# Kernel optimization log

Measured on AMD Instinct MI355X. Metric: run time of the kernel, lower is better.

Reference implementation:

```python
import jax, jax.numpy as jnp
import numpy as np

H = 32          # num attention heads
KVH = 8         # num kv heads
D = 64          # head dim
HID = 2048      # hidden size
MAXB = 1024     # max_bias_length
BASE = 10000.0  # rope theta


def _rope(x, pos):
    # x: (B, S, h, D), pos: (S,) -- GPT-NeoX half-split rotary
    half = D // 2
    inv_freq = 1.0 / (BASE ** (jnp.arange(0, D, 2, dtype=jnp.float32) / D))  # (half,)
    ang = pos[:, None].astype(jnp.float32) * inv_freq                         # (S, half)
    cos = jnp.cos(ang)[None, :, None, :]
    sin = jnp.sin(ang)[None, :, None, :]
    x1, x2 = x[..., :half], x[..., half:]
    return jnp.concatenate([x1 * cos - x2 * sin, x2 * cos + x1 * sin], axis=-1)


def setup_inputs() -> dict:
    key = jax.random.key(0)
    ks = jax.random.split(key, 7)
    B, S = 2, 1024
    hidden_states = jax.random.normal(ks[0], (B, S, HID), dtype=jnp.float32)
    attention_mask = jnp.broadcast_to(
        jnp.tril(jnp.ones((S, S), dtype=jnp.int32))[None, None], (B, 1, S, S))
    # weights stored as (in, out): y = x @ W  (same math as torch Linear)
    Wq = jax.random.normal(ks[1], (HID, H * D), dtype=jnp.float32) * 0.02
    Wk = jax.random.normal(ks[2], (HID, KVH * D), dtype=jnp.float32) * 0.02
    Wv = jax.random.normal(ks[3], (HID, KVH * D), dtype=jnp.float32) * 0.02
    Wo = jax.random.normal(ks[4], (H * D, HID), dtype=jnp.float32) * 0.02
    bias_diag = jax.random.normal(ks[5], (H, MAXB), dtype=jnp.float32) * 0.001
    softmax_offset = jnp.zeros((H,), dtype=jnp.float32)
    return {"hidden_states": hidden_states, "attention_mask": attention_mask,
            "Wq": Wq, "Wk": Wk, "Wv": Wv, "Wo": Wo,
            "bias_diag": bias_diag, "softmax_offset": softmax_offset}


def reference(hidden_states, attention_mask, Wq, Wk, Wv, Wo, bias_diag, softmax_offset):
    B, S, _ = hidden_states.shape
    scaling = D ** (-0.5)
    pos = jnp.arange(S)

    q = (hidden_states @ Wq).reshape(B, S, H, D)
    k = (hidden_states @ Wk).reshape(B, S, KVH, D)
    v = (hidden_states @ Wv).reshape(B, S, KVH, D)

    q = _rope(q, pos)
    k = _rope(k, pos)

    # (B, H, S, D); repeat_kv via repeat on head axis
    q = q.transpose(0, 2, 1, 3)
    k = jnp.repeat(k.transpose(0, 2, 1, 3), H // KVH, axis=1)
    v = jnp.repeat(v.transpose(0, 2, 1, 3), H // KVH, axis=1)

    scores = jnp.einsum('bhqd,bhkd->bhqk', q, k) * scaling

    # learnable diagonal relative-position bias
    rel = pos[:, None] - pos[None, :]                     # (S, S)
    valid = ((rel >= 0) & (rel < MAXB)).astype(scores.dtype)
    idx = jnp.clip(rel, 0, MAXB - 1)
    bias = bias_diag[:, idx] * valid                      # (H, S, S)
    scores = scores + bias[None]

    scores = jnp.where(attention_mask[:, :, :, :S] == 0, -jnp.inf, scores)

    weights = jax.nn.softmax(scores.astype(jnp.float32), axis=-1)

    # adaptive offset subtraction + relu
    offset = jnp.abs(softmax_offset + 1.0)[None, :, None, None]
    num_visible = (pos + 1).astype(jnp.float32)[None, None, :, None]  # along query dim
    weights = jax.nn.relu(weights - offset / num_visible)

    attn_out = jnp.einsum('bhqk,bhkd->bhqd', weights.astype(v.dtype), v)
    attn_out = attn_out.transpose(0, 2, 1, 3).reshape(B, S, H * D)
    return attn_out @ Wo
```

## Files before the change

kernel.cpp:

```cpp
#include <hip/hip_runtime.h>
#include <cstdint>
#include <cstddef>

#define BB   2
#define SS   1024
#define HID  2048
#define HH   32
#define KVHH 8
#define DD   64
#define NQKV 3072
#define QKW  2560

typedef __attribute__((ext_vector_type(8))) short bf16x8;
typedef __attribute__((ext_vector_type(4))) float f32x4;
typedef __attribute__((ext_vector_type(4))) unsigned int u32x4;

__device__ __forceinline__ unsigned short f2bf(float f) {
    unsigned int u = __float_as_uint(f);
    unsigned int r = (u + 0x7fffu + ((u >> 16) & 1u)) >> 16;
    return (unsigned short)r;
}

__device__ __forceinline__ float ex2(float x) {
    float r; asm("v_exp_f32 %0, %1" : "=v"(r) : "v"(x)); return r;
}

__device__ __forceinline__ void g2l16(const unsigned short* g, unsigned short* l) {
    __builtin_amdgcn_global_load_lds(
        (__attribute__((address_space(1))) void*)(unsigned short*)g,
        (__attribute__((address_space(3))) void*)l,
        16, 0, 0);
}

__global__ __launch_bounds__(256) void prep(
    const float* __restrict__ hidden,
    const float* __restrict__ Wq, const float* __restrict__ Wk,
    const float* __restrict__ Wv, const float* __restrict__ Wo,
    unsigned short* __restrict__ hidden_bf,
    unsigned short* __restrict__ WqkvT,
    unsigned short* __restrict__ WoT)
{
    const int z   = blockIdx.z;
    const int tid = threadIdx.x;

    if (z == 4) {
        int r0 = blockIdx.y * 64, c0 = blockIdx.x * 64;
        #pragma unroll
        for (int p = 0; p < 4; ++p) {
            int f = tid + p * 256;
            int row = r0 + (f >> 4), c4 = c0 + (f & 15) * 4;
            float4 v = *(const float4*)&hidden[(size_t)row * 2048 + c4];
            ushort4 o;
            o.x = f2bf(v.x); o.y = f2bf(v.y); o.z = f2bf(v.z); o.w = f2bf(v.w);
            *(ushort4*)&hidden_bf[(size_t)row * 2048 + c4] = o;
        }
        return;
    }

    const float* W;
    unsigned short* Wt;
    int N;
    if (z == 0)      { W = Wq; Wt = WqkvT;                        N = 2048; }
    else if (z == 1) { W = Wk; Wt = WqkvT + (size_t)2048 * 2048;  N = 512;  }
    else if (z == 2) { W = Wv; Wt = WqkvT + (size_t)2560 * 2048;  N = 512;  }
    else             { W = Wo; Wt = WoT;                          N = 2048; }
    if (blockIdx.x * 64 >= N) return;

    __shared__ float t[64][68];
    const int n0 = blockIdx.x * 64, k0 = blockIdx.y * 64;
    #pragma unroll
    for (int p = 0; p < 4; ++p) {
        int f = tid + p * 256;
        int row = f >> 4, c4 = (f & 15) * 4;
        float4 v = *(const float4*)&W[(size_t)(k0 + row) * N + n0 + c4];
        t[row][c4 + 0] = v.x; t[row][c4 + 1] = v.y;
        t[row][c4 + 2] = v.z; t[row][c4 + 3] = v.w;
    }
    __syncthreads();
    #pragma unroll
    for (int p = 0; p < 4; ++p) {
        int f = tid + p * 256;
        int nrow = f >> 4, kc4 = (f & 15) * 4;
        ushort4 o;
        o.x = f2bf(t[kc4 + 0][nrow]);
        o.y = f2bf(t[kc4 + 1][nrow]);
        o.z = f2bf(t[kc4 + 2][nrow]);
        o.w = f2bf(t[kc4 + 3][nrow]);
        *(ushort4*)&Wt[(size_t)(n0 + nrow) * 2048 + k0 + kc4] = o;
    }
}

__global__ __launch_bounds__(256) void gemm_qkv_fused(
    const unsigned short* __restrict__ A,
    const unsigned short* __restrict__ Bt,
    unsigned short* __restrict__ qk_bf,
    unsigned short* __restrict__ v_t)
{
    __shared__ __align__(16) char smem[49152];
    float* Ctf = (float*)smem;

    const int tid  = threadIdx.x;
    const int lane = tid & 63;
    const int wave = tid >> 6;
    const int quad = lane >> 4;
    const int l15  = lane & 15;
    const int wm = (wave >> 1) * 64, wn = (wave & 1) * 32;
    const int m0 = blockIdx.y * 128, n0 = blockIdx.x * 64;
    const int K = 2048;

    f32x4 acc[4][2] = {};

#define STAGE_Q(k0s, buf) do {                                                \
    unsigned short* Ad = (unsigned short*)(smem + (buf) * 24576);             \
    unsigned short* Bd = (unsigned short*)(smem + (buf) * 24576 + 16384);     \
    _Pragma("unroll")                                                         \
    for (int p = 0; p < 4; ++p) {                                             \
        int ci = tid + p * 256;                                               \
        int row_ = ci >> 3, sc_ = (ci & 7) ^ (row_ & 7);                      \
        g2l16(&A[(size_t)(m0 + row_) * K + (k0s) + sc_ * 8], Ad + ci * 8);    \
    }                                                                         \
    _Pragma("unroll")                                                         \
    for (int p = 0; p < 2; ++p) {                                             \
        int ci = tid + p * 256;                                               \
        int row_ = ci >> 3, sc_ = (ci & 7) ^ (row_ & 7);                      \
        g2l16(&Bt[(size_t)(n0 + row_) * K + (k0s) + sc_ * 8], Bd + ci * 8);   \
    } } while (0)

    STAGE_Q(0, 0);
    __syncthreads();
    int cur = 0;
    for (int k0 = 0; k0 < K; k0 += 64) {
        if (k0 + 64 < K) STAGE_Q(k0 + 64, cur ^ 1);
        const short* Ab = (const short*)(smem + cur * 24576);
        const short* Bb = (const short*)(smem + cur * 24576 + 16384);

        #pragma unroll
        for (int s = 0; s < 2; ++s) {
            bf16x8 af[4], bfr[2];
            #pragma unroll
            for (int i = 0; i < 4; ++i) {
                int row = wm + i * 16 + l15;
                af[i] = *(const bf16x8*)(Ab + row * 64 +
                        ((((s << 2) | quad) ^ (row & 7)) * 8));
            }
            #pragma unroll
            for (int j = 0; j < 2; ++j) {
                int row = wn + j * 16 + l15;
                bfr[j] = *(const bf16x8*)(Bb + row * 64 +
                        ((((s << 2) | quad) ^ (row & 7)) * 8));
            }
            #pragma unroll
            for (int i = 0; i < 4; ++i)
                #pragma unroll
                for (int j = 0; j < 2; ++j)
                    acc[i][j] = __builtin_amdgcn_mfma_f32_16x16x32_bf16(
                        af[i], bfr[j], acc[i][j], 0, 0, 0);
        }
        __syncthreads();
        cur ^= 1;
    }

    #pragma unroll
    for (int i = 0; i < 4; ++i)
        #pragma unroll
        for (int j = 0; j < 2; ++j)
            #pragma unroll
            for (int rg = 0; rg < 4; ++rg)
                Ctf[(wm + i * 16 + quad * 4 + rg) * 65 + wn + j * 16 + l15]
                    = acc[i][j][rg];
    __syncthreads();

    const int bx = blockIdx.x;
    const int b  = m0 >> 10;
    const int s0 = m0 & 1023;

    if (bx < 40) {
        const int hc = bx * 64;
        const float scale = (bx < 32) ? 0.18033688011112042f : 1.0f;
        #pragma unroll
        for (int p = 0; p < 4; ++p) {
            int idx = tid + p * 256;
            int row = idx >> 3, t0 = (idx & 7) * 4;
            int s = s0 + row;
            ushort4 o1, o2;
            #pragma unroll
            for (int k = 0; k < 4; ++k) {
                int t = t0 + k;
                float x1 = Ctf[row * 65 + t];
                float x2 = Ctf[row * 65 + t + 32];
                float inv = __expf(-(float)t * 0.28782313662425572f);
                float ang = (float)s * inv;
                float c  = __cosf(ang);
                float sn = __sinf(ang);
                ((unsigned short*)&o1)[k] = f2bf((x1 * c - x2 * sn) * scale);
                ((unsigned short*)&o2)[k] = f2bf((x2 * c + x1 * sn) * scale);
            }
            unsigned short* dst = qk_bf + (size_t)(m0 + row) * QKW + hc;
            *(ushort4*)&dst[t0]      = o1;
            *(ushort4*)&dst[t0 + 32] = o2;
        }
    } else {
        const int vb = b * 512 + (bx - 40) * 64;
        #pragma unroll
        for (int p = 0; p < 8; ++p) {
            int idx = tid + p * 256;
            int c = idx >> 5, srow = (idx & 31) * 4;
            ushort4 o;
            #pragma unroll
            for (int k = 0; k < 4; ++k)
                ((unsigned short*)&o)[k] = f2bf(Ctf[(srow + k) * 65 + c]);
            *(ushort4*)&v_t[(size_t)(vb + c) * 1024 + s0 + srow] = o;
        }
    }
#undef STAGE_Q
}

__global__ __launch_bounds__(256) void gemm_bf16_bt(
    const unsigned short* __restrict__ A,
    const unsigned short* __restrict__ Bt,
    float* __restrict__ C, int M, int N, int K)
{
    __shared__ __align__(16) char smem[49152];

    const int tid  = threadIdx.x;
    const int lane = tid & 63;
    const int wave = tid >> 6;
    const int quad = lane >> 4;
    const int l15  = lane & 15;
    const int wm = (wave >> 1) * 64, wn = (wave & 1) * 32;
    const int m0 = blockIdx.y * 128, n0 = blockIdx.x * 64;

    f32x4 acc[4][2] = {};

#define STAGE_O(k0s, buf) do {                                                \
    unsigned short* Ad = (unsigned short*)(smem + (buf) * 24576);             \
    unsigned short* Bd = (unsigned short*)(smem + (buf) * 24576 + 16384);     \
    _Pragma("unroll")                                                         \
    for (int p = 0; p < 4; ++p) {                                             \
        int ci = tid + p * 256;                                               \
        int row_ = ci >> 3, sc_ = (ci & 7) ^ (row_ & 7);                      \
        g2l16(&A[(size_t)(m0 + row_) * K + (k0s) + sc_ * 8], Ad + ci * 8);    \
    }                                                                         \
    _Pragma("unroll")                                                         \
    for (int p = 0; p < 2; ++p) {                                             \
        int ci = tid + p * 256;                                               \
        int row_ = ci >> 3, sc_ = (ci & 7) ^ (row_ & 7);                      \
        g2l16(&Bt[(size_t)(n0 + row_) * K + (k0s) + sc_ * 8], Bd + ci * 8);   \
    } } while (0)

    STAGE_O(0, 0);
    __syncthreads();
    int cur = 0;
    for (int k0 = 0; k0 < K; k0 += 64) {
        if (k0 + 64 < K) STAGE_O(k0 + 64, cur ^ 1);
        const short* Ab = (const short*)(smem + cur * 24576);
        const short* Bb = (const short*)(smem + cur * 24576 + 16384);

        #pragma unroll
        for (int s = 0; s < 2; ++s) {
            bf16x8 af[4], bfr[2];
            #pragma unroll
            for (int i = 0; i < 4; ++i) {
                int row = wm + i * 16 + l15;
                af[i] = *(const bf16x8*)(Ab + row * 64 +
                        ((((s << 2) | quad) ^ (row & 7)) * 8));
            }
            #pragma unroll
            for (int j = 0; j < 2; ++j) {
                int row = wn + j * 16 + l15;
                bfr[j] = *(const bf16x8*)(Bb + row * 64 +
                        ((((s << 2) | quad) ^ (row & 7)) * 8));
            }
            #pragma unroll
            for (int i = 0; i < 4; ++i)
                #pragma unroll
                for (int j = 0; j < 2; ++j)
                    acc[i][j] = __builtin_amdgcn_mfma_f32_16x16x32_bf16(
                        af[i], bfr[j], acc[i][j], 0, 0, 0);
        }
        __syncthreads();
        cur ^= 1;
    }

    #pragma unroll
    for (int i = 0; i < 4; ++i) {
        int grow = m0 + wm + i * 16 + quad * 4;
        #pragma unroll
        for (int j = 0; j < 2; ++j) {
            int gcol = n0 + wn + j * 16 + l15;
            #pragma unroll
            for (int rg = 0; rg < 4; ++rg)
                C[(size_t)(grow + rg) * N + gcol] = acc[i][j][rg];
        }
    }
#undef STAGE_O
}

__global__ __launch_bounds__(512, 8) void attn_mfma(
    const unsigned short* __restrict__ qk_bf,
    const unsigned short* __restrict__ v_t,
    const float* __restrict__ bias_diag,
    const float* __restrict__ soff,
    unsigned short* __restrict__ AO)
{
    static const unsigned char qtab[16] =
        {15, 14, 13, 12, 10, 11, 8, 9, 4, 5, 6, 7, 1, 0, 3, 2};
    const int id = (int)blockIdx.x;
    const int vq = id >> 8;
    const int c  = id & 255;
    const int qt = qtab[(vq << 2) | (c & 3)];
    const int bh = c >> 2;
    const int h  = bh & 31;
    const int b  = bh >> 5;
    const int kh = h >> 2;
    const int tid  = threadIdx.x;
    const int lane = tid & 63;
    const int wave = tid >> 6;
    const int grp  = wave >> 2;
    const int w4   = wave & 3;
    const int quad = lane >> 4;
    const int l15  = lane & 15;
    const int q0   = qt * 64;

    __shared__ short Ks[2][4096];
    __shared__ short Vs[2][4096];
    __shared__ float bd_s[1024];
    __shared__ float red[2][64];
    float* Fred = (float*)&Ks[0][0];

    for (int i = tid; i < 1024; i += 512)
        bd_s[i] = bias_diag[h * 1024 + i] * 1.4426950408889634f;

    const unsigned short* Kg = qk_bf + (size_t)(b * SS) * QKW + 2048 + kh * 64;
    const unsigned short* Vg = v_t + (size_t)(b * 512 + kh * 64) * SS;

    const int qrow = q0 + w4 * 16 + l15;

    const unsigned short* Qg =
        qk_bf + (size_t)(b * SS + q0 + w4 * 16) * QKW + h * 64;
    bf16x8 qf0 = *(const bf16x8*)(Qg + (size_t)l15 * QKW + quad * 8);
    bf16x8 qf1 = *(const bf16x8*)(Qg + (size_t)l15 * QKW + 32 + quad * 8);

#define STAGE_K(j, buf) do {                                                  \
    int ci = tid;                                                             \
    int row_ = ci >> 3, sc_ = (ci & 7) ^ (row_ & 7);                          \
    g2l16(Kg + (size_t)((j) * 64 + row_) * QKW + sc_ * 8,                     \
          (unsigned short*)&Ks[buf][ci * 8]);                                 \
} while (0)

#define STAGE_V(j, buf) do {                                                  \
    int ci = tid;                                                             \
    int row_ = ci >> 3, sc_ = (ci & 7) ^ (row_ & 7);                          \
    g2l16(Vg + (size_t)row_ * SS + (j) * 64 + sc_ * 8,                        \
          (unsigned short*)&Vs[buf][ci * 8]);                                 \
} while (0)

    float lpa[4] = {0.f, 0.f, 0.f, 0.f};
    STAGE_K(0, 0);
    __syncthreads();
    int cur = 0;
    for (int j = 0; j <= qt; ++j) {
        if (j < qt) STAGE_K(j + 1, cur ^ 1);
        const short* Kb = Ks[cur];
        const bool diag = (j == qt);

        f32x4 acc[2] = {};
        #pragma unroll
        for (int nn = 0; nn < 2; ++nn) {
            int nb = 2 * grp + nn;
            if (diag && nb > w4) continue;
            int row = nb * 16 + l15, sw = row & 7;
            bf16x8 a0 = *(const bf16x8*)(Kb + row * 64 + ((quad ^ sw) * 8));
            bf16x8 a1 = *(const bf16x8*)(Kb + row * 64 + (((quad + 4) ^ sw) * 8));
            acc[nn] = __builtin_amdgcn_mfma_f32_16x16x32_bf16(a0, qf0, acc[nn], 0, 0, 0);
            acc[nn] = __builtin_amdgcn_mfma_f32_16x16x32_bf16(a1, qf1, acc[nn], 0, 0, 0);
        }
        if (!diag) {
            #pragma unroll
            for (int nn = 0; nn < 2; ++nn) {
                int rel0 = qrow - (j * 64 + (2 * grp + nn) * 16 + quad * 4);
                #pragma unroll
                for (int r = 0; r < 4; ++r)
                    lpa[r] += ex2(acc[nn][r] + bd_s[rel0 - r]);
            }
        } else {
            #pragma unroll
            for (int nn = 0; nn < 2; ++nn) {
                int nb = 2 * grp + nn;
                if (nb > w4) continue;
                #pragma unroll
                for (int r = 0; r < 4; ++r) {
                    int rel = qrow - (j * 64 + nb * 16 + quad * 4 + r);
                    if (rel >= 0) lpa[r] += ex2(acc[nn][r] + bd_s[rel]);
                }
            }
        }
        __syncthreads();
        cur ^= 1;
    }

    float lp = (lpa[0] + lpa[1]) + (lpa[2] + lpa[3]);
    lp += __shfl_xor(lp, 16, 64);
    lp += __shfl_xor(lp, 32, 64);
    if (quad == 0) red[grp][w4 * 16 + l15] = lp;
    __syncthreads();
    lp = red[0][w4 * 16 + l15] + red[1][w4 * 16 + l15];
    const float invl = 1.f / lp;
    const float cl   = fabsf(soff[h] + 1.f) / (float)(qrow + 1) * lp;

    f32x4 oacc[4] = {};
    STAGE_K(0, 0);
    STAGE_V(0, 0);
    __syncthreads();
    cur = 0;
    for (int j = 0; j <= qt; ++j) {
        if (j < qt) { STAGE_K(j + 1, cur ^ 1); STAGE_V(j + 1, cur ^ 1); }
        const short* Kb = Ks[cur];
        const short* Vb = Vs[cur];
        const bool diag = (j == qt);

        f32x4 acc[2] = {};
        #pragma unroll
        for (int nn = 0; nn < 2; ++nn) {
            int nb = 2 * grp + nn;
            if (diag && nb > w4) continue;
            int row = nb * 16 + l15, sw = row & 7;
            bf16x8 a0 = *(const bf16x8*)(Kb + row * 64 + ((quad ^ sw) * 8));
            bf16x8 a1 = *(const bf16x8*)(Kb + row * 64 + (((quad + 4) ^ sw) * 8));
            acc[nn] = __builtin_amdgcn_mfma_f32_16x16x32_bf16(a0, qf0, acc[nn], 0, 0, 0);
            acc[nn] = __builtin_amdgcn_mfma_f32_16x16x32_bf16(a1, qf1, acc[nn], 0, 0, 0);
        }

        unsigned int pk[2][2];
        if (!diag) {
            #pragma unroll
            for (int nn = 0; nn < 2; ++nn) {
                float w[4];
                int rel0 = qrow - (j * 64 + (2 * grp + nn) * 16 + quad * 4);
                #pragma unroll
                for (int r = 0; r < 4; ++r)
                    w[r] = fmaxf(ex2(acc[nn][r] + bd_s[rel0 - r]) - cl, 0.f);
                asm("v_cvt_pk_bf16_f32 %0, %1, %2" : "=v"(pk[nn][0]) : "v"(w[0]), "v"(w[1]));
                asm("v_cvt_pk_bf16_f32 %0, %1, %2" : "=v"(pk[nn][1]) : "v"(w[2]), "v"(w[3]));
            }
        } else {
            #pragma unroll
            for (int nn = 0; nn < 2; ++nn) {
                int nb = 2 * grp + nn;
                float w[4];
                #pragma unroll
                for (int r = 0; r < 4; ++r) {
                    int rel = qrow - (j * 64 + nb * 16 + quad * 4 + r);
                    float e = 0.f;
                    if (rel >= 0)
                        e = fmaxf(ex2(acc[nn][r] + bd_s[rel]) - cl, 0.f);
                    w[r] = e;
                }
                asm("v_cvt_pk_bf16_f32 %0, %1, %2" : "=v"(pk[nn][0]) : "v"(w[0]), "v"(w[1]));
                asm("v_cvt_pk_bf16_f32 %0, %1, %2" : "=v"(pk[nn][1]) : "v"(w[2]), "v"(w[3]));
            }
        }
        unsigned int ppk[2][2];
        #pragma unroll
        for (int nn = 0; nn < 2; ++nn) {
            ppk[nn][0] = __shfl_xor(pk[nn][0], 16, 64);
            ppk[nn][1] = __shfl_xor(pk[nn][1], 16, 64);
        }

        if (!(diag && grp == 1 && w4 < 2)) {
            const bool oddq = quad & 1;
            const int  cv   = ((quad & 1) << 1) | (quad >> 1);
            unsigned int w0 = oddq ? ppk[1][0] : pk[0][0];
            unsigned int w1 = oddq ? ppk[1][1] : pk[0][1];
            unsigned int w2 = oddq ? pk[1][0]  : ppk[0][0];
            unsigned int w3 = oddq ? pk[1][1]  : ppk[0][1];
            u32x4 t; t[0] = w0; t[1] = w1; t[2] = w2; t[3] = w3;
            bf16x8 pf = __builtin_bit_cast(bf16x8, t);
            #pragma unroll
            for (int nd = 0; nd < 4; ++nd) {
                int rowv = nd * 16 + l15, swv = rowv & 7;
                bf16x8 vf = *(const bf16x8*)(Vb + rowv * 64 + (((cv + 4 * grp) ^ swv) * 8));
                oacc[nd] = __builtin_amdgcn_mfma_f32_16x16x32_bf16(pf, vf, oacc[nd], 0, 0, 0);
            }
        }
        __syncthreads();
        cur ^= 1;
    }

    if (grp == 1) {
        #pragma unroll
        for (int nd = 0; nd < 4; ++nd)
            #pragma unroll
            for (int r = 0; r < 4; ++r)
                Fred[(w4 * 16 + quad * 4 + r) * 64 + nd * 16 + l15] = oacc[nd][r];
    }
    __syncthreads();
    if (grp == 0) {
        float invl_r[4];
        #pragma unroll
        for (int r = 0; r < 4; ++r)
            invl_r[r] = __shfl(invl, quad * 4 + r, 64);
        unsigned short* aop =
            AO + (size_t)(b * SS + q0 + w4 * 16 + quad * 4) * 2048 + h * 64 + l15;
        #pragma unroll
        for (int nd = 0; nd < 4; ++nd)
            #pragma unroll
            for (int r = 0; r < 4; ++r) {
                float o = (oacc[nd][r] +
                           Fred[(w4 * 16 + quad * 4 + r) * 64 + nd * 16 + l15])
                          * invl_r[r];
                aop[(size_t)r * 2048 + nd * 16] = f2bf(o);
            }
    }
#undef STAGE_K
#undef STAGE_V
}

extern "C" void kernel_launch(void* const* d_in, const int* in_sizes, int n_in,
                              void* d_out, int out_size, void* d_ws, size_t ws_size,
                              hipStream_t stream)
{
    const float* hidden    = (const float*)d_in[0];
    const float* Wq        = (const float*)d_in[2];
    const float* Wk        = (const float*)d_in[3];
    const float* Wv        = (const float*)d_in[4];
    const float* Wo        = (const float*)d_in[5];
    const float* bias_diag = (const float*)d_in[6];
    const float* soff      = (const float*)d_in[7];
    float* out = (float*)d_out;

    char* wsb = (char*)d_ws;
    unsigned short* hidden_bf = (unsigned short*)wsb;
    unsigned short* WqkvT     = (unsigned short*)(wsb + (size_t)8388608);
    unsigned short* AO_bf     = (unsigned short*)(wsb + (size_t)12582912);
    unsigned short* WoT       = (unsigned short*)(wsb + (size_t)20971520);
    unsigned short* qk_bf     = (unsigned short*)(wsb + (size_t)29360128);
    unsigned short* v_t       = (unsigned short*)(wsb + (size_t)29360128 + (size_t)2048 * 2560 * 2);

    prep<<<dim3(32, 32, 5), dim3(256), 0, stream>>>(
        hidden, Wq, Wk, Wv, Wo, hidden_bf, WqkvT, WoT);

    gemm_qkv_fused<<<dim3(48, 16), dim3(256), 0, stream>>>(
        hidden_bf, WqkvT, qk_bf, v_t);

    attn_mfma<<<dim3(1024), dim3(512), 0, stream>>>(
        qk_bf, v_t, bias_diag, soff, AO_bf);

    gemm_bf16_bt<<<dim3(2048 / 64, 2048 / 128), dim3(256), 0, stream>>>(
        AO_bf, WoT, out, 2048, 2048, 2048);
}
```

Measured before the change: 197.1 us.

## Use persistent attention blocks with atomic work queue and MFMA priority hints

Converts the attention kernel into a persistent kernel with 768 blocks that pull work items from a global atomic counter. The counter is reset by the prep kernel. Items are ordered longest query tile first, so the causal triangle balances dynamically instead of relying on a static interleave table. It also wraps the MFMA sections in s_setprio and lowers the launch-bounds occupancy hint from 8 to 6. The cost is extra barriers and an atomic per item, and correctness now depends on the reset in prep running before every launch.

Result: slower. 207.4 us (+5.3%).

```diff
diff --git a/kernel.cpp b/kernel.cpp
--- a/kernel.cpp
+++ b/kernel.cpp
@@ -38,12 +38,14 @@
     const float* __restrict__ Wv, const float* __restrict__ Wo,
     unsigned short* __restrict__ hidden_bf,
     unsigned short* __restrict__ WqkvT,
-    unsigned short* __restrict__ WoT)
+    unsigned short* __restrict__ WoT,
+    unsigned int* __restrict__ ctr)
 {
     const int z   = blockIdx.z;
     const int tid = threadIdx.x;
 
     if (z == 4) {
+        if (blockIdx.x == 0 && blockIdx.y == 0 && tid == 0) *ctr = 0u;
         int r0 = blockIdx.y * 64, c0 = blockIdx.x * 64;
         #pragma unroll
         for (int p = 0; p < 4; ++p) {
@@ -296,23 +298,14 @@
 #undef STAGE_O
 }
 
-__global__ __launch_bounds__(512, 8) void attn_mfma(
+__global__ __launch_bounds__(512, 6) void attn_mfma(
     const unsigned short* __restrict__ qk_bf,
     const unsigned short* __restrict__ v_t,
     const float* __restrict__ bias_diag,
     const float* __restrict__ soff,
-    unsigned short* __restrict__ AO)
+    unsigned short* __restrict__ AO,
+    unsigned int* __restrict__ ctr)
 {
-    static const unsigned char qtab[16] =
-        {15, 14, 13, 12, 10, 11, 8, 9, 4, 5, 6, 7, 1, 0, 3, 2};
-    const int id = (int)blockIdx.x;
-    const int vq = id >> 8;
-    const int c  = id & 255;
-    const int qt = qtab[(vq << 2) | (c & 3)];
-    const int bh = c >> 2;
-    const int h  = bh & 31;
-    const int b  = bh >> 5;
-    const int kh = h >> 2;
     const int tid  = threadIdx.x;
     const int lane = tid & 63;
     const int wave = tid >> 6;
@@ -320,26 +313,13 @@
     const int w4   = wave & 3;
     const int quad = lane >> 4;
     const int l15  = lane & 15;
-    const int q0   = qt * 64;
 
     __shared__ short Ks[2][4096];
     __shared__ short Vs[2][4096];
     __shared__ float bd_s[1024];
     __shared__ float red[2][64];
+    __shared__ int item_s;
     float* Fred = (float*)&Ks[0][0];
-
-    for (int i = tid; i < 1024; i += 512)
-        bd_s[i] = bias_diag[h * 1024 + i] * 1.4426950408889634f;
-
-    const unsigned short* Kg = qk_bf + (size_t)(b * SS) * QKW + 2048 + kh * 64;
-    const unsigned short* Vg = v_t + (size_t)(b * 512 + kh * 64) * SS;
-
-    const int qrow = q0 + w4 * 16 + l15;
-
-    const unsigned short* Qg =
-        qk_bf + (size_t)(b * SS + q0 + w4 * 16) * QKW + h * 64;
-    bf16x8 qf0 = *(const bf16x8*)(Qg + (size_t)l15 * QKW + quad * 8);
-    bf16x8 qf1 = *(const bf16x8*)(Qg + (size_t)l15 * QKW + 32 + quad * 8);
 
 #define STAGE_K(j, buf) do {                                                  \
     int ci = tid;                                                             \
@@ -355,162 +335,196 @@
           (unsigned short*)&Vs[buf][ci * 8]);                                 \
 } while (0)
 
-    float lpa[4] = {0.f, 0.f, 0.f, 0.f};
-    STAGE_K(0, 0);
-    __syncthreads();
-    int cur = 0;
-    for (int j = 0; j <= qt; ++j) {
-        if (j < qt) STAGE_K(j + 1, cur ^ 1);
-        const short* Kb = Ks[cur];
-        const bool diag = (j == qt);
-
-        f32x4 acc[2] = {};
-        #pragma unroll
-        for (int nn = 0; nn < 2; ++nn) {
-            int nb = 2 * grp + nn;
-            if (diag && nb > w4) continue;
-            int row = nb * 16 + l15, sw = row & 7;
-            bf16x8 a0 = *(const bf16x8*)(Kb + row * 64 + ((quad ^ sw) * 8));
-            bf16x8 a1 = *(const bf16x8*)(Kb + row * 64 + (((quad + 4) ^ sw) * 8));
-            acc[nn] = __builtin_amdgcn_mfma_f32_16x16x32_bf16(a0, qf0, acc[nn], 0, 0, 0);
-            acc[nn] = __builtin_amdgcn_mfma_f32_16x16x32_bf16(a1, qf1, acc[nn], 0, 0, 0);
-        }
-        if (!diag) {
-            #pragma unroll
-            for (int nn = 0; nn < 2; ++nn) {
-                int rel0 = qrow - (j * 64 + (2 * grp + nn) * 16 + quad * 4);
-                #pragma unroll
-                for (int r = 0; r < 4; ++r)
-                    lpa[r] += ex2(acc[nn][r] + bd_s[rel0 - r]);
-            }
-        } else {
+    for (;;) {
+        if (tid == 0) item_s = (int)atomicAdd(ctr, 1u);
+        __syncthreads();
+        const int item = item_s;
+        if (item >= 1024) break;
+
+        const int qt = 15 - (item >> 6);
+        const int hb = item & 63;
+        const int h  = hb & 31;
+        const int b  = hb >> 5;
+        const int kh = h >> 2;
+        const int q0 = qt * 64;
+
+        for (int i = tid; i < 1024; i += 512)
+            bd_s[i] = bias_diag[h * 1024 + i] * 1.4426950408889634f;
+
+        const unsigned short* Kg = qk_bf + (size_t)(b * SS) * QKW + 2048 + kh * 64;
+        const unsigned short* Vg = v_t + (size_t)(b * 512 + kh * 64) * SS;
+
+        const int qrow = q0 + w4 * 16 + l15;
+
+        const unsigned short* Qg =
+            qk_bf + (size_t)(b * SS + q0 + w4 * 16) * QKW + h * 64;
+        bf16x8 qf0 = *(const bf16x8*)(Qg + (size_t)l15 * QKW + quad * 8);
+        bf16x8 qf1 = *(const bf16x8*)(Qg + (size_t)l15 * QKW + 32 + quad * 8);
+
+        float lpa[4] = {0.f, 0.f, 0.f, 0.f};
+        STAGE_K(0, 0);
+        __syncthreads();
+        int cur = 0;
+        for (int j = 0; j <= qt; ++j) {
+            if (j < qt) STAGE_K(j + 1, cur ^ 1);
+            const short* Kb = Ks[cur];
+            const bool diag = (j == qt);
+
+            f32x4 acc[2] = {};
+            __builtin_amdgcn_s_setprio(1);
             #pragma unroll
             for (int nn = 0; nn < 2; ++nn) {
                 int nb = 2 * grp + nn;
-                if (nb > w4) continue;
-                #pragma unroll
-                for (int r = 0; r < 4; ++r) {
-                    int rel = qrow - (j * 64 + nb * 16 + quad * 4 + r);
-                    if (rel >= 0) lpa[r] += ex2(acc[nn][r] + bd_s[rel]);
+                if (diag && nb > w4) continue;
+                int row = nb * 16 + l15, sw = row & 7;
+                bf16x8 a0 = *(const bf16x8*)(Kb + row * 64 + ((quad ^ sw) * 8));
+                bf16x8 a1 = *(const bf16x8*)(Kb + row * 64 + (((quad + 4) ^ sw) * 8));
+                acc[nn] = __builtin_amdgcn_mfma_f32_16x16x32_bf16(a0, qf0, acc[nn], 0, 0, 0);
+                acc[nn] = __builtin_amdgcn_mfma_f32_16x16x32_bf16(a1, qf1, acc[nn], 0, 0, 0);
+            }
+            __builtin_amdgcn_s_setprio(0);
+            if (!diag) {
+                #pragma unroll
+                for (int nn = 0; nn < 2; ++nn) {
+                    int rel0 = qrow - (j * 64 + (2 * grp + nn) * 16 + quad * 4);
+                    #pragma unroll
+                    for (int r = 0; r < 4; ++r)
+                        lpa[r] += ex2(acc[nn][r] + bd_s[rel0 - r]);
                 }
-            }
-        }
-        __syncthreads();
-        cur ^= 1;
-    }
-
-    float lp = (lpa[0] + lpa[1]) + (lpa[2] + lpa[3]);
-    lp += __shfl_xor(lp, 16, 64);
-    lp += __shfl_xor(lp, 32, 64);
-    if (quad == 0) red[grp][w4 * 16 + l15] = lp;
-    __syncthreads();
-    lp = red[0][w4 * 16 + l15] + red[1][w4 * 16 + l15];
-    const float invl = 1.f / lp;
-    const float cl   = fabsf(soff[h] + 1.f) / (float)(qrow + 1) * lp;
-
-    f32x4 oacc[4] = {};
-    STAGE_K(0, 0);
-    STAGE_V(0, 0);
-    __syncthreads();
-    cur = 0;
-    for (int j = 0; j <= qt; ++j) {
-        if (j < qt) { STAGE_K(j + 1, cur ^ 1); STAGE_V(j + 1, cur ^ 1); }
-        const short* Kb = Ks[cur];
-        const short* Vb = Vs[cur];
-        const bool diag = (j == qt);
-
-        f32x4 acc[2] = {};
-        #pragma unroll
-        for (int nn = 0; nn < 2; ++nn) {
-            int nb = 2 * grp + nn;
-            if (diag && nb > w4) continue;
-            int row = nb * 16 + l15, sw = row & 7;
-            bf16x8 a0 = *(const bf16x8*)(Kb + row * 64 + ((quad ^ sw) * 8));
-            bf16x8 a1 = *(const bf16x8*)(Kb + row * 64 + (((quad + 4) ^ sw) * 8));
-            acc[nn] = __builtin_amdgcn_mfma_f32_16x16x32_bf16(a0, qf0, acc[nn], 0, 0, 0);
-            acc[nn] = __builtin_amdgcn_mfma_f32_16x16x32_bf16(a1, qf1, acc[nn], 0, 0, 0);
-        }
-
-        unsigned int pk[2][2];
-        if (!diag) {
-            #pragma unroll
-            for (int nn = 0; nn < 2; ++nn) {
-                float w[4];
-                int rel0 = qrow - (j * 64 + (2 * grp + nn) * 16 + quad * 4);
-                #pragma unroll
-                for (int r = 0; r < 4; ++r)
-                    w[r] = fmaxf(ex2(acc[nn][r] + bd_s[rel0 - r]) - cl, 0.f);
-                asm("v_cvt_pk_bf16_f32 %0, %1, %2" : "=v"(pk[nn][0]) : "v"(w[0]), "v"(w[1]));
-                asm("v_cvt_pk_bf16_f32 %0, %1, %2" : "=v"(pk[nn][1]) : "v"(w[2]), "v"(w[3]));
-            }
-        } else {
+            } else {
+                #pragma unroll
+                for (int nn = 0; nn < 2; ++nn) {
+                    int nb = 2 * grp + nn;
+                    if (nb > w4) continue;
+                    #pragma unroll
+                    for (int r = 0; r < 4; ++r) {
+                        int rel = qrow - (j * 64 + nb * 16 + quad * 4 + r);
+                        if (rel >= 0) lpa[r] += ex2(acc[nn][r] + bd_s[rel]);
+                    }
+                }
+            }
+            __syncthreads();
+            cur ^= 1;
+        }
+
+        float lp = (lpa[0] + lpa[1]) + (lpa[2] + lpa[3]);
+        lp += __shfl_xor(lp, 16, 64);
+        lp += __shfl_xor(lp, 32, 64);
+        if (quad == 0) red[grp][w4 * 16 + l15] = lp;
+        __syncthreads();
+        lp = red[0][w4 * 16 + l15] + red[1][w4 * 16 + l15];
+        const float invl = 1.f / lp;
+        const float cl   = fabsf(soff[h] + 1.f) / (float)(qrow + 1) * lp;
+
+        f32x4 oacc[4] = {};
+        STAGE_K(0, 0);
+        STAGE_V(0, 0);
+        __syncthreads();
+        cur = 0;
+        for (int j = 0; j <= qt; ++j) {
+            if (j < qt) { STAGE_K(j + 1, cur ^ 1); STAGE_V(j + 1, cur ^ 1); }
+            const short* Kb = Ks[cur];
+            const short* Vb = Vs[cur];
+            const bool diag = (j == qt);
+
+            f32x4 acc[2] = {};
+            __builtin_amdgcn_s_setprio(1);
             #pragma unroll
             for (int nn = 0; nn < 2; ++nn) {
                 int nb = 2 * grp + nn;
-                float w[4];
+                if (diag && nb > w4) continue;
+                int row = nb * 16 + l15, sw = row & 7;
+                bf16x8 a0 = *(const bf16x8*)(Kb + row * 64 + ((quad ^ sw) * 8));
+                bf16x8 a1 = *(const bf16x8*)(Kb + row * 64 + (((quad + 4) ^ sw) * 8));
+                acc[nn] = __builtin_amdgcn_mfma_f32_16x16x32_bf16(a0, qf0, acc[nn], 0, 0, 0);
+                acc[nn] = __builtin_amdgcn_mfma_f32_16x16x32_bf16(a1, qf1, acc[nn], 0, 0, 0);
+            }
+            __builtin_amdgcn_s_setprio(0);
+
+            unsigned int pk[2][2];
+            if (!diag) {
+                #pragma unroll
+                for (int nn = 0; nn < 2; ++nn) {
+                    float w[4];
+                    int rel0 = qrow - (j * 64 + (2 * grp + nn) * 16 + quad * 4);
+                    #pragma unroll
+                    for (int r = 0; r < 4; ++r)
+                        w[r] = fmaxf(ex2(acc[nn][r] + bd_s[rel0 - r]) - cl, 0.f);
+                    asm("v_cvt_pk_bf16_f32 %0, %1, %2" : "=v"(pk[nn][0]) : "v"(w[0]), "v"(w[1]));
+                    asm("v_cvt_pk_bf16_f32 %0, %1, %2" : "=v"(pk[nn][1]) : "v"(w[2]), "v"(w[3]));
+                }
+            } else {
+                #pragma unroll
+                for (int nn = 0; nn < 2; ++nn) {
+                    int nb = 2 * grp + nn;
+                    float w[4];
+                    #pragma unroll
+                    for (int r = 0; r < 4; ++r) {
+                        int rel = qrow - (j * 64 + nb * 16 + quad * 4 + r);
+                        float e = 0.f;
+                        if (rel >= 0)
+                            e = fmaxf(ex2(acc[nn][r] + bd_s[rel]) - cl, 0.f);
+                        w[r] = e;
+                    }
+                    asm("v_cvt_pk_bf16_f32 %0, %1, %2" : "=v"(pk[nn][0]) : "v"(w[0]), "v"(w[1]));
+                    asm("v_cvt_pk_bf16_f32 %0, %1, %2" : "=v"(pk[nn][1]) : "v"(w[2]), "v"(w[3]));
+                }
+            }
+            unsigned int ppk[2][2];
+            #pragma unroll
+            for (int nn = 0; nn < 2; ++nn) {
+                ppk[nn][0] = __shfl_xor(pk[nn][0], 16, 64);
+                ppk[nn][1] = __shfl_xor(pk[nn][1], 16, 64);
+            }
+
+            if (!(diag && grp == 1 && w4 < 2)) {
+                const bool oddq = quad & 1;
+                const int  cv   = ((quad & 1) << 1) | (quad >> 1);
+                unsigned int w0 = oddq ? ppk[1][0] : pk[0][0];
+                unsigned int w1 = oddq ? ppk[1][1] : pk[0][1];
+                unsigned int w2 = oddq ? pk[1][0]  : ppk[0][0];
+                unsigned int w3 = oddq ? pk[1][1]  : ppk[0][1];
+                u32x4 t; t[0] = w0; t[1] = w1; t[2] = w2; t[3] = w3;
+                bf16x8 pf = __builtin_bit_cast(bf16x8, t);
+                __builtin_amdgcn_s_setprio(1);
+                #pragma unroll
+                for (int nd = 0; nd < 4; ++nd) {
+                    int rowv = nd * 16 + l15, swv = rowv & 7;
+                    bf16x8 vf = *(const bf16x8*)(Vb + rowv * 64 + (((cv + 4 * grp) ^ swv) * 8));
+                    oacc[nd] = __builtin_amdgcn_mfma_f32_16x16x32_bf16(pf, vf, oacc[nd], 0, 0, 0);
+                }
+                __builtin_amdgcn_s_setprio(0);
+            }
+            __syncthreads();
+            cur ^= 1;
+        }
+
+        if (grp == 1) {
+            #pragma unroll
+            for (int nd = 0; nd < 4; ++nd)
+                #pragma unroll
+                for (int r = 0; r < 4; ++r)
+                    Fred[(w4 * 16 + quad * 4 + r) * 64 + nd * 16 + l15] = oacc[nd][r];
+        }
+        __syncthreads();
+        if (grp == 0) {
+            float invl_r[4];
+            #pragma unroll
+            for (int r = 0; r < 4; ++r)
+                invl_r[r] = __shfl(invl, quad * 4 + r, 64);
+            unsigned short* aop =
+                AO + (size_t)(b * SS + q0 + w4 * 16 + quad * 4) * 2048 + h * 64 + l15;
+            #pragma unroll
+            for (int nd = 0; nd < 4; ++nd)
                 #pragma unroll
                 for (int r = 0; r < 4; ++r) {
-                    int rel = qrow - (j * 64 + nb * 16 + quad * 4 + r);
-                    float e = 0.f;
-                    if (rel >= 0)
-                        e = fmaxf(ex2(acc[nn][r] + bd_s[rel]) - cl, 0.f);
-                    w[r] = e;
+                    float o = (oacc[nd][r] +
+                               Fred[(w4 * 16 + quad * 4 + r) * 64 + nd * 16 + l15])
+                              * invl_r[r];
+                    aop[(size_t)r * 2048 + nd * 16] = f2bf(o);
                 }
-                asm("v_cvt_pk_bf16_f32 %0, %1, %2" : "=v"(pk[nn][0]) : "v"(w[0]), "v"(w[1]));
-                asm("v_cvt_pk_bf16_f32 %0, %1, %2" : "=v"(pk[nn][1]) : "v"(w[2]), "v"(w[3]));
-            }
-        }
-        unsigned int ppk[2][2];
-        #pragma unroll
-        for (int nn = 0; nn < 2; ++nn) {
-            ppk[nn][0] = __shfl_xor(pk[nn][0], 16, 64);
-            ppk[nn][1] = __shfl_xor(pk[nn][1], 16, 64);
-        }
-
-        if (!(diag && grp == 1 && w4 < 2)) {
-            const bool oddq = quad & 1;
-            const int  cv   = ((quad & 1) << 1) | (quad >> 1);
-            unsigned int w0 = oddq ? ppk[1][0] : pk[0][0];
-            unsigned int w1 = oddq ? ppk[1][1] : pk[0][1];
-            unsigned int w2 = oddq ? pk[1][0]  : ppk[0][0];
-            unsigned int w3 = oddq ? pk[1][1]  : ppk[0][1];
-            u32x4 t; t[0] = w0; t[1] = w1; t[2] = w2; t[3] = w3;
-            bf16x8 pf = __builtin_bit_cast(bf16x8, t);
-            #pragma unroll
-            for (int nd = 0; nd < 4; ++nd) {
-                int rowv = nd * 16 + l15, swv = rowv & 7;
-                bf16x8 vf = *(const bf16x8*)(Vb + rowv * 64 + (((cv + 4 * grp) ^ swv) * 8));
-                oacc[nd] = __builtin_amdgcn_mfma_f32_16x16x32_bf16(pf, vf, oacc[nd], 0, 0, 0);
-            }
-        }
-        __syncthreads();
-        cur ^= 1;
-    }
-
-    if (grp == 1) {
-        #pragma unroll
-        for (int nd = 0; nd < 4; ++nd)
-            #pragma unroll
-            for (int r = 0; r < 4; ++r)
-                Fred[(w4 * 16 + quad * 4 + r) * 64 + nd * 16 + l15] = oacc[nd][r];
-    }
-    __syncthreads();
-    if (grp == 0) {
-        float invl_r[4];
-        #pragma unroll
-        for (int r = 0; r < 4; ++r)
-            invl_r[r] = __shfl(invl, quad * 4 + r, 64);
-        unsigned short* aop =
-            AO + (size_t)(b * SS + q0 + w4 * 16 + quad * 4) * 2048 + h * 64 + l15;
-        #pragma unroll
-        for (int nd = 0; nd < 4; ++nd)
-            #pragma unroll
-            for (int r = 0; r < 4; ++r) {
-                float o = (oacc[nd][r] +
-                           Fred[(w4 * 16 + quad * 4 + r) * 64 + nd * 16 + l15])
-                          * invl_r[r];
-                aop[(size_t)r * 2048 + nd * 16] = f2bf(o);
-            }
+        }
+        __syncthreads();
     }
 #undef STAGE_K
 #undef STAGE_V
@@ -536,15 +550,16 @@
     unsigned short* WoT       = (unsigned short*)(wsb + (size_t)20971520);
     unsigned short* qk_bf     = (unsigned short*)(wsb + (size_t)29360128);
     unsigned short* v_t       = (unsigned short*)(wsb + (size_t)29360128 + (size_t)2048 * 2560 * 2);
+    unsigned int*   ctr       = (unsigned int*)(wsb + (size_t)41943040);
 
     prep<<<dim3(32, 32, 5), dim3(256), 0, stream>>>(
-        hidden, Wq, Wk, Wv, Wo, hidden_bf, WqkvT, WoT);
+        hidden, Wq, Wk, Wv, Wo, hidden_bf, WqkvT, WoT, ctr);
 
     gemm_qkv_fused<<<dim3(48, 16), dim3(256), 0, stream>>>(
         hidden_bf, WqkvT, qk_bf, v_t);
 
-    attn_mfma<<<dim3(1024), dim3(512), 0, stream>>>(
-        qk_bf, v_t, bias_diag, soff, AO_bf);
+    attn_mfma<<<dim3(768), dim3(512), 0, stream>>>(
+        qk_bf, v_t, bias_diag, soff, AO_bf, ctr);
 
     gemm_bf16_bt<<<dim3(2048 / 64, 2048 / 128), dim3(256), 0, stream>>>(
         AO_bf, WoT, out, 2048, 2048, 2048);
```
